# Kernel tuning notes

Measured on AMD Instinct MI355X. Metric: run time of the kernel, lower is better.

## Reference

```python
import jax, jax.numpy as jnp
import numpy as np

HIDDEN_DIM = 1024
SEQ_LEN = 4096
D_IN = 1024


def setup_inputs() -> dict:
    key = jax.random.key(0)
    ks = jax.random.split(key, 9)
    s = 1.0 / np.sqrt(D_IN)
    return {
        "q": jax.random.normal(ks[0], (SEQ_LEN, D_IN), jnp.float32),
        "k": jax.random.normal(ks[1], (SEQ_LEN, D_IN), jnp.float32),
        "v": jax.random.normal(ks[2], (SEQ_LEN, D_IN), jnp.float32),
        "Wq": jax.random.normal(ks[3], (D_IN, HIDDEN_DIM), jnp.float32) * s,
        "bq": jnp.zeros((HIDDEN_DIM,), jnp.float32),
        "Wk": jax.random.normal(ks[4], (D_IN, HIDDEN_DIM), jnp.float32) * s,
        "bk": jnp.zeros((HIDDEN_DIM,), jnp.float32),
        "Wv": jax.random.normal(ks[5], (D_IN, HIDDEN_DIM), jnp.float32) * s,
        "bv": jnpp_zeros() if False else jnp.zeros((HIDDEN_DIM,), jnp.float32),
    }


def reference(q, k, v, Wq, bq, Wk, bk, Wv, bv):
    # Dense projections (flax Dense: x @ W + b)
    query = q @ Wq + bq          # [S, H]
    key_p = k @ Wk + bk          # [S, H]
    value = v @ Wv + bv          # [S, H]
    # scores = Q K^T / sqrt(hidden_dim)  -> [S, S]
    scores = jnp.matmul(query, key_p.T) / jnp.sqrt(jnp.float32(HIDDEN_DIM))
    weights = jax.nn.softmax(scores, axis=-1)
    context = jnp.matmul(weights, value)  # [S, H]
    return context
```

## Files before the change

### kernel.cpp

```cpp
#include <hip/hip_runtime.h>


typedef short short4v __attribute__((ext_vector_type(4)));
typedef short short8  __attribute__((ext_vector_type(8)));
typedef float f32x4   __attribute__((ext_vector_type(4)));

#define MFMA16 __builtin_amdgcn_mfma_f32_16x16x32_bf16

__device__ __forceinline__ short f2bf(float f) {
    union { float f; unsigned u; } x; x.f = f;
    unsigned r = (x.u + 0x7FFFu + ((x.u >> 16) & 1u)) >> 16;
    return (short)r;
}
__device__ __forceinline__ float bf2f(short s) {
    union { unsigned u; float f; } x;
    x.u = ((unsigned)(unsigned short)s) << 16; return x.f;
}
__device__ __forceinline__ void store_out(short* p, float v) { *p = f2bf(v); }
__device__ __forceinline__ void store_out(float* p, float v) { *p = v; }

__device__ __forceinline__ void gl2lds(const short* g, short* l) {
    __builtin_amdgcn_global_load_lds(
        (const __attribute__((address_space(1))) void*)g,
        (__attribute__((address_space(3))) void*)l, 16, 0, 0);
}

__global__ __launch_bounds__(256) void prep_all(
    const float* __restrict__ W0, const float* __restrict__ W1,
    const float* __restrict__ W2, short* __restrict__ Wt,
    const float* __restrict__ q, const float* __restrict__ k,
    const float* __restrict__ v, short* __restrict__ xb)
{
    const int z = blockIdx.z;
    if (z < 3) {
        __shared__ float tile[64][65];
        const float* W = z == 0 ? W0 : (z == 1 ? W1 : W2);
        short* T = Wt + (size_t)z * 1048576;
        const int c0 = blockIdx.x * 64;
        const int r0 = blockIdx.y * 64;
        const int tx = threadIdx.x & 63;
        const int ty = threadIdx.x >> 6;
        #pragma unroll
        for (int p = 0; p < 16; ++p) {
            int r = ty + p * 4;
            tile[r][tx] = W[(size_t)(r0 + r) * 1024 + c0 + tx];
        }
        __syncthreads();
        #pragma unroll
        for (int p = 0; p < 16; ++p) {
            int r = ty + p * 4;
            T[(size_t)(c0 + r) * 1024 + r0 + tx] = f2bf(tile[tx][r]);
        }
    } else {
        const float* src = z == 3 ? q : (z == 4 ? k : v);
        short* dst = xb + (size_t)(z - 3) * 4194304;
        const int blk = blockIdx.y * 16 + blockIdx.x;
        for (int i = blk * 256 + threadIdx.x; i < 1048576; i += 256 * 256) {
            float4 f = ((const float4*)src)[i];
            short4v o;
            o[0] = f2bf(f.x); o[1] = f2bf(f.y);
            o[2] = f2bf(f.z); o[3] = f2bf(f.w);
            ((short4v*)dst)[i] = o;
        }
    }
}

template <typename TOut, int MODE, int SK = 1>
__global__ __launch_bounds__(256) void gemm64(
    const short* __restrict__ A, const short* __restrict__ Bt,
    const float* __restrict__ b0, const float* __restrict__ b1,
    const float* __restrict__ b2, TOut* __restrict__ C,
    float* __restrict__ Cout, short* __restrict__ Vt,
    int M, int N, int Kd, int lda, int ldb, float scale, int kiters)
{
    constexpr int LDSN = (MODE == 1) ? (128 * 136) : (128 * 64 * 2);
    __shared__ short Lds[LDSN];
    short* As = Lds;
    short* Bs = Lds + 128 * 64;

    const int t    = threadIdx.x;
    const int lane = t & 63;
    const int wv   = t >> 6;

    const int nb  = gridDim.x;
    const int bid = blockIdx.y * nb + blockIdx.x;
    const int band   = bid / (8 * nb);
    const int within = bid - band * 8 * nb;
    const int m0 = (band * 8 + (within & 7)) * 128;
    const int n0 = (within >> 3) * 128;

    const float* bias = nullptr;
    int kbeg = 0;
    int myk  = kiters;
    float* Cw = nullptr;
    if constexpr (MODE == 1) {
        const int z = blockIdx.z;
        A  += (size_t)z * M * lda;
        Bt += (size_t)z * N * ldb;
        C  += (size_t)z * M * N;
        bias = z == 0 ? b0 : (z == 1 ? b1 : b2);
    }
    if constexpr (MODE == 2) {
        const int z = blockIdx.z;
        kbeg = z * kiters * 64;
        if (z == SK - 1) {
            myk = (Kd >> 6) - (SK - 1) * kiters;
            Cw  = Cout;
        } else {
            Cw = (float*)C + (size_t)z * M * N;
        }
    }
    (void)b0; (void)b1; (void)b2; (void)Cout;

    const int sr = lane >> 3;
    const int sc = (lane & 7) ^ sr;
    const short* pA = A  + (size_t)(m0 + wv * 32 + sr) * lda + kbeg + sc * 8;
    const short* pB = Bt + (size_t)(n0 + wv * 32 + sr) * ldb + kbeg + sc * 8;
    const size_t a8 = (size_t)8 * lda;
    const size_t b8 = (size_t)8 * ldb;
    short* lA = As + wv * 2048;
    short* lB = Bs + wv * 2048;

    const int wm = wv & 1, wn = wv >> 1;
    const int lr = lane & 15, lq = lane >> 4;
    const int xkey = lr & 7;

    f32x4 acc[4][4];
    #pragma unroll
    for (int i = 0; i < 4; ++i)
        #pragma unroll
        for (int j = 0; j < 4; ++j) {
            f32x4 z = {0.f, 0.f, 0.f, 0.f};
            acc[i][j] = z;
        }

    for (int kk = 0; kk < myk; ++kk) {
        #pragma unroll
        for (int r = 0; r < 4; ++r) gl2lds(pA + r * a8, lA + r * 512);
        #pragma unroll
        for (int r = 0; r < 4; ++r) gl2lds(pB + r * b8, lB + r * 512);
        pA += 64; pB += 64;
        __syncthreads();

        #pragma unroll
        for (int h = 0; h < 2; ++h) {
            short8 af[4], bfr[4];
            #pragma unroll
            for (int i = 0; i < 4; ++i)
                af[i] = *(const short8*)
                    &As[(wm * 64 + i * 16 + lr) * 64 + (((h * 4 + lq) ^ xkey) * 8)];
            #pragma unroll
            for (int j = 0; j < 4; ++j)
                bfr[j] = *(const short8*)
                    &Bs[(wn * 64 + j * 16 + lr) * 64 + (((h * 4 + lq) ^ xkey) * 8)];
            #pragma unroll
            for (int i = 0; i < 4; ++i)
                #pragma unroll
                for (int j = 0; j < 4; ++j)
                    acc[i][j] = MFMA16(af[i], bfr[j], acc[i][j], 0, 0, 0);
        }
        __syncthreads();
    }

    if constexpr (MODE == 1) {
        if (blockIdx.z == 2) {
            #pragma unroll
            for (int i = 0; i < 4; ++i) {
                #pragma unroll
                for (int j = 0; j < 4; ++j) {
                    const int colL = wn * 64 + j * 16 + lr;
                    const float bb = bias[n0 + colL];
                    #pragma unroll
                    for (int r = 0; r < 4; ++r) {
                        const int rowL = wm * 64 + i * 16 + lq * 4 + r;
                        Lds[colL * 136 + rowL] = f2bf(acc[i][j][r] * scale + bb);
                    }
                }
            }
            __syncthreads();
            const int c = t >> 1, part = t & 1;
            short* dst = Vt + (size_t)(n0 + c) * 4096 + m0 + part * 64;
            #pragma unroll
            for (int s = 0; s < 8; ++s)
                *(short8*)(dst + s * 8) =
                    *(const short8*)&Lds[c * 136 + part * 64 + s * 8];
            return;
        }
    }
    #pragma unroll
    for (int i = 0; i < 4; ++i) {
        #pragma unroll
        for (int j = 0; j < 4; ++j) {
            const int crow = m0 + wm * 64 + i * 16 + lq * 4;
            const int ccol = n0 + wn * 64 + j * 16 + lr;
            float bb = 0.f;
            if constexpr (MODE == 1) bb = bias[ccol];
            #pragma unroll
            for (int r = 0; r < 4; ++r) {
                const float val = acc[i][j][r] * scale + bb;
                if constexpr (MODE == 2)
                    Cw[(size_t)(crow + r) * N + ccol] = val;
                else
                    store_out(&C[(size_t)(crow + r) * N + ccol], val);
            }
        }
    }
}

__global__ __launch_bounds__(256) void softmax_bf16(short* __restrict__ S)
{
    const int row = blockIdx.x;
    short8* r8 = (short8*)(S + (size_t)row * 4096);
    const int t = threadIdx.x;

    float x[16];
    #pragma unroll
    for (int i = 0; i < 2; ++i) {
        short8 raw = r8[t + 256 * i];
        #pragma unroll
        for (int j = 0; j < 8; ++j) x[8 * i + j] = bf2f(raw[j]);
    }
    float m = -1e30f;
    #pragma unroll
    for (int i = 0; i < 16; ++i) m = fmaxf(m, x[i]);
    #pragma unroll
    for (int off = 32; off > 0; off >>= 1) m = fmaxf(m, __shfl_xor(m, off));

    __shared__ float redm[4], reds[4];
    const int wv = t >> 6;
    if ((t & 63) == 0) redm[wv] = m;
    __syncthreads();
    m = fmaxf(fmaxf(redm[0], redm[1]), fmaxf(redm[2], redm[3]));

    float s = 0.f;
    #pragma unroll
    for (int i = 0; i < 16; ++i) { x[i] = __expf(x[i] - m); s += x[i]; }
    #pragma unroll
    for (int off = 32; off > 0; off >>= 1) s += __shfl_xor(s, off);
    if ((t & 63) == 0) reds[wv] = s;
    __syncthreads();
    s = reds[0] + reds[1] + reds[2] + reds[3];
    const float inv = 1.f / s;

    #pragma unroll
    for (int i = 0; i < 2; ++i) {
        short8 o;
        #pragma unroll
        for (int j = 0; j < 8; ++j) o[j] = f2bf(x[8 * i + j] * inv);
        r8[t + 256 * i] = o;
    }
}

__global__ __launch_bounds__(256) void combine3(
    const float* __restrict__ p0, const float* __restrict__ p1,
    float* __restrict__ out)
{
    for (int i = blockIdx.x * 256 + threadIdx.x; i < 1048576; i += 256 * 1024) {
        float4 a = ((const float4*)p0)[i];
        float4 b = ((const float4*)p1)[i];
        float4 o = ((const float4*)out)[i];
        o.x += a.x + b.x; o.y += a.y + b.y;
        o.z += a.z + b.z; o.w += a.w + b.w;
        ((float4*)out)[i] = o;
    }
}

extern "C" void kernel_launch(void* const* d_in, const int* in_sizes, int n_in,
                              void* d_out, int out_size, void* d_ws, size_t ws_size,
                              hipStream_t stream)
{
    const float* q  = (const float*)d_in[0];
    const float* k  = (const float*)d_in[1];
    const float* v  = (const float*)d_in[2];
    const float* Wq = (const float*)d_in[3];
    const float* bq = (const float*)d_in[4];
    const float* Wk = (const float*)d_in[5];
    const float* bk = (const float*)d_in[6];
    const float* Wv = (const float*)d_in[7];
    const float* bv = (const float*)d_in[8];
    float* out = (float*)d_out;

    char* ws = (char*)d_ws;
    const size_t MB = 1ull << 20;
    short* Wt = (short*)(ws + 0);
    short* xb = (short*)(ws + 6 * MB);
    short* pr = (short*)(ws + 30 * MB);
    short* Vt = (short*)(ws + 46 * MB);
    short* S  = (short*)(ws + 54 * MB);
    float* pp = (float*)(ws + 0);

    prep_all<<<dim3(16, 16, 6), 256, 0, stream>>>(Wq, Wk, Wv, Wt, q, k, v, xb);
    gemm64<short, 1><<<dim3(8, 32, 3), 256, 0, stream>>>(
        xb, Wt, bq, bk, bv, pr, nullptr, Vt,
        4096, 1024, 1024, 1024, 1024, 1.f, 16);
    gemm64<short, 0><<<dim3(32, 32), 256, 0, stream>>>(
        pr, pr + 4194304, nullptr, nullptr, nullptr, S, nullptr, nullptr,
        4096, 4096, 1024, 1024, 1024, 0.03125f, 16);
    softmax_bf16<<<4096, 256, 0, stream>>>(S);
    gemm64<float, 2, 3><<<dim3(8, 32, 3), 256, 0, stream>>>(
        S, Vt, nullptr, nullptr, nullptr, pp, out, nullptr,
        4096, 1024, 4096, 4096, 4096, 1.f, 21);
    combine3<<<1024, 256, 0, stream>>>(pp, pp + 4194304, out);
}
```

Before: 270.5 us.

## Fuse softmax into QK^T epilogue and normalize inside split-K PV GEMM

The standalone softmax kernel is removed. The QK^T GEMM epilogue now writes exp(score) in bf16 directly and accumulates per-row sums into a workspace vector with atomics. The PV GEMM then divides by the row sum in its epilogue and atomically adds its split-K partials into the output, which the prep kernel now zeroes; this also removes the partial buffers and the combine kernel. The aim is to cut a full read/write pass over the score matrix and the partial-sum traffic. In exchange, the max subtraction is dropped, so large scores could overflow, and many scalar float atomics are added.

```diff
diff --git a/kernel.cpp b/kernel.cpp
--- a/kernel.cpp
+++ b/kernel.cpp
@@ -29,7 +29,8 @@
     const float* __restrict__ W0, const float* __restrict__ W1,
     const float* __restrict__ W2, short* __restrict__ Wt,
     const float* __restrict__ q, const float* __restrict__ k,
-    const float* __restrict__ v, short* __restrict__ xb)
+    const float* __restrict__ v, short* __restrict__ xb,
+    float* __restrict__ outz, float* __restrict__ lz)
 {
     const int z = blockIdx.z;
     if (z < 3) {
@@ -51,7 +52,7 @@
             int r = ty + p * 4;
             T[(size_t)(c0 + r) * 1024 + r0 + tx] = f2bf(tile[tx][r]);
         }
-    } else {
+    } else if (z < 6) {
         const float* src = z == 3 ? q : (z == 4 ? k : v);
         short* dst = xb + (size_t)(z - 3) * 4194304;
         const int blk = blockIdx.y * 16 + blockIdx.x;
@@ -62,15 +63,22 @@
             o[2] = f2bf(f.z); o[3] = f2bf(f.w);
             ((short4v*)dst)[i] = o;
         }
-    }
-}
-
-template <typename TOut, int MODE, int SK = 1>
+    } else {
+        const int blk = blockIdx.y * 16 + blockIdx.x;
+        const int tid = blk * 256 + threadIdx.x;
+        float4 zv = {0.f, 0.f, 0.f, 0.f};
+        for (int i = tid; i < 1048576; i += 65536)
+            ((float4*)outz)[i] = zv;
+        if (tid < 4096) lz[tid] = 0.f;
+    }
+}
+
+template <typename TOut, int MODE, int EPI, int SK = 1>
 __global__ __launch_bounds__(256) void gemm64(
     const short* __restrict__ A, const short* __restrict__ Bt,
     const float* __restrict__ b0, const float* __restrict__ b1,
     const float* __restrict__ b2, TOut* __restrict__ C,
-    float* __restrict__ Cout, short* __restrict__ Vt,
+    float* __restrict__ aux, short* __restrict__ Vt,
     int M, int N, int Kd, int lda, int ldb, float scale, int kiters)
 {
     constexpr int LDSN = (MODE == 1) ? (128 * 136) : (128 * 64 * 2);
@@ -92,7 +100,6 @@
     const float* bias = nullptr;
     int kbeg = 0;
     int myk  = kiters;
-    float* Cw = nullptr;
     if constexpr (MODE == 1) {
         const int z = blockIdx.z;
         A  += (size_t)z * M * lda;
@@ -103,14 +110,9 @@
     if constexpr (MODE == 2) {
         const int z = blockIdx.z;
         kbeg = z * kiters * 64;
-        if (z == SK - 1) {
-            myk = (Kd >> 6) - (SK - 1) * kiters;
-            Cw  = Cout;
-        } else {
-            Cw = (float*)C + (size_t)z * M * N;
-        }
-    }
-    (void)b0; (void)b1; (void)b2; (void)Cout;
+        if (z == SK - 1) myk = (Kd >> 6) - (SK - 1) * kiters;
+    }
+    (void)b0; (void)b1; (void)b2;
 
     const int sr = lane >> 3;
     const int sc = (lane & 7) ^ sr;
@@ -187,6 +189,57 @@
             return;
         }
     }
+
+    if constexpr (EPI == 1) {
+        float psum[4][4];
+        #pragma unroll
+        for (int i = 0; i < 4; ++i)
+            #pragma unroll
+            for (int r = 0; r < 4; ++r) psum[i][r] = 0.f;
+        #pragma unroll
+        for (int i = 0; i < 4; ++i) {
+            #pragma unroll
+            for (int j = 0; j < 4; ++j) {
+                const int crow = m0 + wm * 64 + i * 16 + lq * 4;
+                const int ccol = n0 + wn * 64 + j * 16 + lr;
+                #pragma unroll
+                for (int r = 0; r < 4; ++r) {
+                    const float e = __expf(acc[i][j][r] * scale);
+                    psum[i][r] += e;
+                    C[(size_t)(crow + r) * N + ccol] = f2bf(e);
+                }
+            }
+        }
+        #pragma unroll
+        for (int i = 0; i < 4; ++i) {
+            #pragma unroll
+            for (int r = 0; r < 4; ++r) {
+                float s = psum[i][r];
+                s += __shfl_xor(s, 1); s += __shfl_xor(s, 2);
+                s += __shfl_xor(s, 4); s += __shfl_xor(s, 8);
+                if (lr == 0)
+                    atomicAdd(&aux[m0 + wm * 64 + i * 16 + lq * 4 + r], s);
+            }
+        }
+        return;
+    }
+    if constexpr (EPI == 2) {
+        #pragma unroll
+        for (int i = 0; i < 4; ++i) {
+            #pragma unroll
+            for (int r = 0; r < 4; ++r) {
+                const int crow = m0 + wm * 64 + i * 16 + lq * 4 + r;
+                const float inv = 1.f / aux[crow];
+                #pragma unroll
+                for (int j = 0; j < 4; ++j) {
+                    const int ccol = n0 + wn * 64 + j * 16 + lr;
+                    atomicAdd((float*)&C[(size_t)crow * N + ccol],
+                              acc[i][j][r] * inv);
+                }
+            }
+        }
+        return;
+    }
     #pragma unroll
     for (int i = 0; i < 4; ++i) {
         #pragma unroll
@@ -196,72 +249,10 @@
             float bb = 0.f;
             if constexpr (MODE == 1) bb = bias[ccol];
             #pragma unroll
-            for (int r = 0; r < 4; ++r) {
-                const float val = acc[i][j][r] * scale + bb;
-                if constexpr (MODE == 2)
-                    Cw[(size_t)(crow + r) * N + ccol] = val;
-                else
-                    store_out(&C[(size_t)(crow + r) * N + ccol], val);
-            }
-        }
-    }
-}
-
-__global__ __launch_bounds__(256) void softmax_bf16(short* __restrict__ S)
-{
-    const int row = blockIdx.x;
-    short8* r8 = (short8*)(S + (size_t)row * 4096);
-    const int t = threadIdx.x;
-
-    float x[16];
-    #pragma unroll
-    for (int i = 0; i < 2; ++i) {
-        short8 raw = r8[t + 256 * i];
-        #pragma unroll
-        for (int j = 0; j < 8; ++j) x[8 * i + j] = bf2f(raw[j]);
-    }
-    float m = -1e30f;
-    #pragma unroll
-    for (int i = 0; i < 16; ++i) m = fmaxf(m, x[i]);
-    #pragma unroll
-    for (int off = 32; off > 0; off >>= 1) m = fmaxf(m, __shfl_xor(m, off));
-
-    __shared__ float redm[4], reds[4];
-    const int wv = t >> 6;
-    if ((t & 63) == 0) redm[wv] = m;
-    __syncthreads();
-    m = fmaxf(fmaxf(redm[0], redm[1]), fmaxf(redm[2], redm[3]));
-
-    float s = 0.f;
-    #pragma unroll
-    for (int i = 0; i < 16; ++i) { x[i] = __expf(x[i] - m); s += x[i]; }
-    #pragma unroll
-    for (int off = 32; off > 0; off >>= 1) s += __shfl_xor(s, off);
-    if ((t & 63) == 0) reds[wv] = s;
-    __syncthreads();
-    s = reds[0] + reds[1] + reds[2] + reds[3];
-    const float inv = 1.f / s;
-
-    #pragma unroll
-    for (int i = 0; i < 2; ++i) {
-        short8 o;
-        #pragma unroll
-        for (int j = 0; j < 8; ++j) o[j] = f2bf(x[8 * i + j] * inv);
-        r8[t + 256 * i] = o;
-    }
-}
-
-__global__ __launch_bounds__(256) void combine3(
-    const float* __restrict__ p0, const float* __restrict__ p1,
-    float* __restrict__ out)
-{
-    for (int i = blockIdx.x * 256 + threadIdx.x; i < 1048576; i += 256 * 1024) {
-        float4 a = ((const float4*)p0)[i];
-        float4 b = ((const float4*)p1)[i];
-        float4 o = ((const float4*)out)[i];
-        o.x += a.x + b.x; o.y += a.y + b.y;
-        o.z += a.z + b.z; o.w += a.w + b.w;
-        ((float4*)out)[i] = o;
+            for (int r = 0; r < 4; ++r)
+                store_out(&C[(size_t)(crow + r) * N + ccol],
+                          acc[i][j][r] * scale + bb);
+        }
     }
 }
 
@@ -287,18 +278,17 @@
     short* pr = (short*)(ws + 30 * MB);
     short* Vt = (short*)(ws + 46 * MB);
     short* S  = (short*)(ws + 54 * MB);
-    float* pp = (float*)(ws + 0);
-
-    prep_all<<<dim3(16, 16, 6), 256, 0, stream>>>(Wq, Wk, Wv, Wt, q, k, v, xb);
-    gemm64<short, 1><<<dim3(8, 32, 3), 256, 0, stream>>>(
+    float* l  = (float*)(ws + 86 * MB);
+
+    prep_all<<<dim3(16, 16, 7), 256, 0, stream>>>(
+        Wq, Wk, Wv, Wt, q, k, v, xb, out, l);
+    gemm64<short, 1, 0><<<dim3(8, 32, 3), 256, 0, stream>>>(
         xb, Wt, bq, bk, bv, pr, nullptr, Vt,
         4096, 1024, 1024, 1024, 1024, 1.f, 16);
-    gemm64<short, 0><<<dim3(32, 32), 256, 0, stream>>>(
-        pr, pr + 4194304, nullptr, nullptr, nullptr, S, nullptr, nullptr,
+    gemm64<short, 0, 1><<<dim3(32, 32), 256, 0, stream>>>(
+        pr, pr + 4194304, nullptr, nullptr, nullptr, S, l, nullptr,
         4096, 4096, 1024, 1024, 1024, 0.03125f, 16);
-    softmax_bf16<<<4096, 256, 0, stream>>>(S);
-    gemm64<float, 2, 3><<<dim3(8, 32, 3), 256, 0, stream>>>(
-        S, Vt, nullptr, nullptr, nullptr, pp, out, nullptr,
+    gemm64<float, 2, 2, 3><<<dim3(8, 32, 3), 256, 0, stream>>>(
+        S, Vt, nullptr, nullptr, nullptr, out, l, nullptr,
         4096, 1024, 4096, 4096, 4096, 1.f, 21);
-    combine3<<<1024, 256, 0, stream>>>(pp, pp + 4194304, out);
-}
+}
```

Measured after the change: 300.5 us. +11.1%, slower.
